# Kernel tuning notes

Hardware: AMD Instinct MI355X
Metric: run time of the kernel (lower is better)

The kernel has to match this reference:

```python
import jax, jax.numpy as jnp
import numpy as np

N_NODES = 50000
N_EDGES = 800000
D = 128


def gcn_conv(x, W, b, src, dst, num_nodes):
    """PyG GCNConv: x @ W, add self-loops, symmetric normalization, scatter-add, + bias."""
    x = x @ W  # [N, out]
    loop = jnp.arange(num_nodes, dtype=src.dtype)
    s = jnp.concatenate([src, loop])  # [E+N]
    d = jnp.concatenate([dst, loop])
    w = jnp.ones(s.shape[0], x.dtype)  # edge_weight=None -> ones (self-loop fill=1)
    deg = jax.ops.segment_sum(w, d, num_segments=num_nodes)  # [N]
    dinv = jnp.where(deg > 0, jax.lax.rsqrt(deg), 0.0)
    norm = dinv[s] * dinv[d]  # [E+N]
    out = jax.ops.segment_sum(x[s] * norm[:, None], d, num_segments=num_nodes)
    return out + b


def setup_inputs() -> dict:
    key = jax.random.key(0)
    ks = jax.random.split(key, 8)
    sc = 1.0 / np.sqrt(D)
    x = jax.random.normal(ks[0], (N_NODES, D), dtype=jnp.float32)
    edge_index = jax.random.randint(ks[1], (2, N_EDGES), 0, N_NODES)
    W1 = jax.random.normal(ks[2], (D, D), dtype=jnp.float32) * sc
    W2 = jax.random.normal(ks[3], (D, D), dtype=jnp.float32) * sc
    W3 = jax.random.normal(ks[4], (D, D), dtype=jnp.float32) * sc
    b1 = jnp.zeros((D,), jnp.float32)
    b2 = jnp.zeros((D,), jnp.float32)
    b3 = jnp.zeros((D,), jnp.float32)
    return {"x": x, "edge_index": edge_index, "W1": W1, "b1": b1,
            "W2": W2, "b2": b2, "W3": W3, "b3": b3}


def reference(x, edge_index, W1, b1, W2, b2, W3, b3):
    src, dst = edge_index[0], edge_index[1]
    n = x.shape[0]
    x = jax.nn.relu(gcn_conv(x, W1, b1, src, dst, n))
    x = jax.nn.relu(gcn_conv(x, W2, b2, src, dst, n))
    return gcn_conv(x, W3, b3, src, dst, n)
```

## Files before the change

kernel.cpp:

```cpp
#include <hip/hip_runtime.h>
#include <hip/hip_fp16.h>
#include <math.h>

#define D 128

typedef __attribute__((ext_vector_type(8))) _Float16 half8;
typedef __attribute__((ext_vector_type(4))) float f32x4;


__global__ void count_rank_kernel(const int* __restrict__ dst, int* __restrict__ cnt,
                                  int* __restrict__ rank, int E) {
    int e0 = (blockIdx.x * blockDim.x + threadIdx.x) * 8;
    if (e0 + 7 < E) {
        int4 da = *(const int4*)(dst + e0);
        int4 db = *(const int4*)(dst + e0 + 4);
        int4 ra, rb;
        ra.x = atomicAdd(&cnt[da.x], 1);
        ra.y = atomicAdd(&cnt[da.y], 1);
        ra.z = atomicAdd(&cnt[da.z], 1);
        ra.w = atomicAdd(&cnt[da.w], 1);
        rb.x = atomicAdd(&cnt[db.x], 1);
        rb.y = atomicAdd(&cnt[db.y], 1);
        rb.z = atomicAdd(&cnt[db.z], 1);
        rb.w = atomicAdd(&cnt[db.w], 1);
        *(int4*)(rank + e0)     = ra;
        *(int4*)(rank + e0 + 4) = rb;
    } else {
        for (int e = e0; e < E; ++e) rank[e] = atomicAdd(&cnt[dst[e]], 1);
    }
}

__global__ __launch_bounds__(1024) void scan_kernel(const int* __restrict__ cnt,
                                                    int* __restrict__ rowptr,
                                                    float* __restrict__ dinv,
                                                    int N) {
    __shared__ int wsum[16];
    __shared__ int carry_s;
    int tid  = threadIdx.x;
    int lane = tid & 63;
    int wid  = tid >> 6;
    if (tid == 0) carry_s = 0;
    __syncthreads();
    for (int base = 0; base < N; base += 4096) {
        int i = base + tid * 4;
        int4 v = make_int4(0, 0, 0, 0);
        if (i + 3 < N) v = *(const int4*)(cnt + i);
        else {
            if (i + 0 < N) v.x = cnt[i + 0];
            if (i + 1 < N) v.y = cnt[i + 1];
            if (i + 2 < N) v.z = cnt[i + 2];
            if (i + 3 < N) v.w = cnt[i + 3];
        }
        int s0 = v.x, s1 = s0 + v.y, s2 = s1 + v.z, s3 = s2 + v.w;
        int sc = s3;
        #pragma unroll
        for (int off = 1; off < 64; off <<= 1) {
            int t = __shfl_up(sc, off, 64);
            if (lane >= off) sc += t;
        }
        if (lane == 63) wsum[wid] = sc;
        __syncthreads();
        if (tid < 16) {
            int w = wsum[tid];
            #pragma unroll
            for (int off = 1; off < 16; off <<= 1) {
                int t = __shfl_up(w, off, 64);
                if (tid >= off) w += t;
            }
            wsum[tid] = w;
        }
        __syncthreads();
        int waveoff = (wid > 0) ? wsum[wid - 1] : 0;
        int excl = carry_s + waveoff + (sc - s3);
        if (i + 0 < N) { rowptr[i + 0] = excl;      dinv[i + 0] = rsqrtf((float)v.x + 1.0f); }
        if (i + 1 < N) { rowptr[i + 1] = excl + s0; dinv[i + 1] = rsqrtf((float)v.y + 1.0f); }
        if (i + 2 < N) { rowptr[i + 2] = excl + s1; dinv[i + 2] = rsqrtf((float)v.z + 1.0f); }
        if (i + 3 < N) { rowptr[i + 3] = excl + s2; dinv[i + 3] = rsqrtf((float)v.w + 1.0f); }
        __syncthreads();
        if (tid == 0) carry_s += wsum[15];
        __syncthreads();
    }
    if (tid == 0) rowptr[N] = carry_s;
}

__global__ void fill_kernel(const int* __restrict__ src, const int* __restrict__ dst,
                            const int* __restrict__ rank, const int* __restrict__ rowptr,
                            int* __restrict__ col, int E) {
    int e0 = (blockIdx.x * blockDim.x + threadIdx.x) * 8;
    if (e0 + 7 < E) {
        int4 da = *(const int4*)(dst + e0);
        int4 db = *(const int4*)(dst + e0 + 4);
        int4 ra = *(const int4*)(rank + e0);
        int4 rb = *(const int4*)(rank + e0 + 4);
        int4 sa = *(const int4*)(src + e0);
        int4 sb = *(const int4*)(src + e0 + 4);
        int p0 = rowptr[da.x] + ra.x;
        int p1 = rowptr[da.y] + ra.y;
        int p2 = rowptr[da.z] + ra.z;
        int p3 = rowptr[da.w] + ra.w;
        int p4 = rowptr[db.x] + rb.x;
        int p5 = rowptr[db.y] + rb.y;
        int p6 = rowptr[db.z] + rb.z;
        int p7 = rowptr[db.w] + rb.w;
        col[p0] = sa.x; col[p1] = sa.y; col[p2] = sa.z; col[p3] = sa.w;
        col[p4] = sb.x; col[p5] = sb.y; col[p6] = sb.z; col[p7] = sb.w;
    } else {
        for (int e = e0; e < E; ++e) col[rowptr[dst[e]] + rank[e]] = src[e];
    }
}


__global__ void convw_kernel(const float* __restrict__ W1, const float* __restrict__ W2,
                             const float* __restrict__ W3, __half* __restrict__ WhT) {
    int i = blockIdx.x * blockDim.x + threadIdx.x;
    int l = i >> 14;
    int j = i & 16383;
    int n = j >> 7, k = j & 127;
    const float* W = (l == 0) ? W1 : (l == 1) ? W2 : W3;
    WhT[(size_t)i] = __float2half(W[(size_t)k * D + n]);
}


__global__ __launch_bounds__(256) void gemm_mfma_f32(const float* __restrict__ X,
                                                     const __half* __restrict__ WhT,
                                                     const float* __restrict__ dinv,
                                                     __half* __restrict__ Y, int M) {
    int tid  = threadIdx.x;
    int wave = tid >> 6;
    int lane = tid & 63;
    int quad = lane >> 4;
    int l16  = lane & 15;
    int m0   = blockIdx.x * 64 + wave * 16;
    if (m0 >= M) return;

    f32x4 acc[8];
    #pragma unroll
    for (int t = 0; t < 8; ++t) acc[t] = (f32x4)0.0f;

    const float* xrow = X + (size_t)(m0 + l16) * D;

    #pragma unroll
    for (int ks = 0; ks < 4; ++ks) {
        int k0 = ks * 32 + quad * 8;
        float4 x0 = *(const float4*)(xrow + k0);
        float4 x1 = *(const float4*)(xrow + k0 + 4);
        half8 a;
        a[0] = (_Float16)x0.x; a[1] = (_Float16)x0.y;
        a[2] = (_Float16)x0.z; a[3] = (_Float16)x0.w;
        a[4] = (_Float16)x1.x; a[5] = (_Float16)x1.y;
        a[6] = (_Float16)x1.z; a[7] = (_Float16)x1.w;
        #pragma unroll
        for (int t = 0; t < 8; ++t) {
            half8 b = *(const half8*)(WhT + (size_t)(t * 16 + l16) * D + k0);
            acc[t] = __builtin_amdgcn_mfma_f32_16x16x32_f16(a, b, acc[t], 0, 0, 0);
        }
    }

    float4 dv = *(const float4*)(dinv + m0 + quad * 4);
    float dvs[4] = {dv.x, dv.y, dv.z, dv.w};
    #pragma unroll
    for (int t = 0; t < 8; ++t) {
        #pragma unroll
        for (int r = 0; r < 4; ++r) {
            int grow = m0 + quad * 4 + r;
            Y[(size_t)grow * D + t * 16 + l16] = __float2half(acc[t][r] * dvs[r]);
        }
    }
}

__global__ __launch_bounds__(256) void gemm_mfma_f16(const __half* __restrict__ Xh,
                                                     const __half* __restrict__ WhT,
                                                     const float* __restrict__ dinv,
                                                     __half* __restrict__ Y, int M) {
    int tid  = threadIdx.x;
    int wave = tid >> 6;
    int lane = tid & 63;
    int quad = lane >> 4;
    int l16  = lane & 15;
    int m0   = blockIdx.x * 64 + wave * 16;
    if (m0 >= M) return;

    f32x4 acc[8];
    #pragma unroll
    for (int t = 0; t < 8; ++t) acc[t] = (f32x4)0.0f;

    const __half* xrow = Xh + (size_t)(m0 + l16) * D;

    #pragma unroll
    for (int ks = 0; ks < 4; ++ks) {
        int k0 = ks * 32 + quad * 8;
        half8 a = *(const half8*)(xrow + k0);
        #pragma unroll
        for (int t = 0; t < 8; ++t) {
            half8 b = *(const half8*)(WhT + (size_t)(t * 16 + l16) * D + k0);
            acc[t] = __builtin_amdgcn_mfma_f32_16x16x32_f16(a, b, acc[t], 0, 0, 0);
        }
    }

    float4 dv = *(const float4*)(dinv + m0 + quad * 4);
    float dvs[4] = {dv.x, dv.y, dv.z, dv.w};
    #pragma unroll
    for (int t = 0; t < 8; ++t) {
        #pragma unroll
        for (int r = 0; r < 4; ++r) {
            int grow = m0 + quad * 4 + r;
            Y[(size_t)grow * D + t * 16 + l16] = __float2half(acc[t][r] * dvs[r]);
        }
    }
}


#define GATHER(vv, cc) __half2 vv = ((const __half2*)(ys + (size_t)(cc) * D))[lane]

template <bool FINAL>
__global__ __launch_bounds__(256) void aggregate_kernel(const __half* __restrict__ ys,
                                                        const int* __restrict__ rowptr,
                                                        const int* __restrict__ col,
                                                        const float* __restrict__ dinv,
                                                        const float* __restrict__ b,
                                                        __half* __restrict__ outh,
                                                        float* __restrict__ outf,
                                                        int N) {
    int gwave = (blockIdx.x * blockDim.x + threadIdx.x) >> 6;
    int lane  = threadIdx.x & 63;
    if (gwave >= N) return;
    int row = gwave;
    int s = rowptr[row], e = rowptr[row + 1];

    __half2 hself = ((const __half2*)(ys + (size_t)row * D))[lane];
    float2 a0 = __half22float2(hself);
    float2 a1 = make_float2(0.f, 0.f), a2 = make_float2(0.f, 0.f),
           a3 = make_float2(0.f, 0.f), a4 = make_float2(0.f, 0.f),
           a5 = make_float2(0.f, 0.f), a6 = make_float2(0.f, 0.f),
           a7 = make_float2(0.f, 0.f);

    for (int base = s; base < e; base += 64) {
        int idx = base + lane;
        int myc = (idx < e) ? col[idx] : 0;
        int nb  = min(64, e - base);
        int j = 0;
        for (; j + 16 <= nb; j += 16) {
            int c0 = __shfl(myc, j + 0),  c1 = __shfl(myc, j + 1);
            int c2 = __shfl(myc, j + 2),  c3 = __shfl(myc, j + 3);
            int c4 = __shfl(myc, j + 4),  c5 = __shfl(myc, j + 5);
            int c6 = __shfl(myc, j + 6),  c7 = __shfl(myc, j + 7);
            int c8 = __shfl(myc, j + 8),  c9 = __shfl(myc, j + 9);
            int cA = __shfl(myc, j + 10), cB = __shfl(myc, j + 11);
            int cC = __shfl(myc, j + 12), cD = __shfl(myc, j + 13);
            int cE = __shfl(myc, j + 14), cF = __shfl(myc, j + 15);
            GATHER(v0, c0); GATHER(v1, c1); GATHER(v2, c2); GATHER(v3, c3);
            GATHER(v4, c4); GATHER(v5, c5); GATHER(v6, c6); GATHER(v7, c7);
            GATHER(v8, c8); GATHER(v9, c9); GATHER(vA, cA); GATHER(vB, cB);
            GATHER(vC, cC); GATHER(vD, cD); GATHER(vE, cE); GATHER(vF, cF);
            a0.x += __low2float(v0); a0.y += __high2float(v0);
            a1.x += __low2float(v1); a1.y += __high2float(v1);
            a2.x += __low2float(v2); a2.y += __high2float(v2);
            a3.x += __low2float(v3); a3.y += __high2float(v3);
            a4.x += __low2float(v4); a4.y += __high2float(v4);
            a5.x += __low2float(v5); a5.y += __high2float(v5);
            a6.x += __low2float(v6); a6.y += __high2float(v6);
            a7.x += __low2float(v7); a7.y += __high2float(v7);
            a0.x += __low2float(v8); a0.y += __high2float(v8);
            a1.x += __low2float(v9); a1.y += __high2float(v9);
            a2.x += __low2float(vA); a2.y += __high2float(vA);
            a3.x += __low2float(vB); a3.y += __high2float(vB);
            a4.x += __low2float(vC); a4.y += __high2float(vC);
            a5.x += __low2float(vD); a5.y += __high2float(vD);
            a6.x += __low2float(vE); a6.y += __high2float(vE);
            a7.x += __low2float(vF); a7.y += __high2float(vF);
        }
        for (; j + 8 <= nb; j += 8) {
            int c0 = __shfl(myc, j + 0), c1 = __shfl(myc, j + 1);
            int c2 = __shfl(myc, j + 2), c3 = __shfl(myc, j + 3);
            int c4 = __shfl(myc, j + 4), c5 = __shfl(myc, j + 5);
            int c6 = __shfl(myc, j + 6), c7 = __shfl(myc, j + 7);
            GATHER(v0, c0); GATHER(v1, c1); GATHER(v2, c2); GATHER(v3, c3);
            GATHER(v4, c4); GATHER(v5, c5); GATHER(v6, c6); GATHER(v7, c7);
            a0.x += __low2float(v0); a0.y += __high2float(v0);
            a1.x += __low2float(v1); a1.y += __high2float(v1);
            a2.x += __low2float(v2); a2.y += __high2float(v2);
            a3.x += __low2float(v3); a3.y += __high2float(v3);
            a4.x += __low2float(v4); a4.y += __high2float(v4);
            a5.x += __low2float(v5); a5.y += __high2float(v5);
            a6.x += __low2float(v6); a6.y += __high2float(v6);
            a7.x += __low2float(v7); a7.y += __high2float(v7);
        }
        for (; j + 4 <= nb; j += 4) {
            int c0 = __shfl(myc, j + 0), c1 = __shfl(myc, j + 1);
            int c2 = __shfl(myc, j + 2), c3 = __shfl(myc, j + 3);
            GATHER(v0, c0); GATHER(v1, c1); GATHER(v2, c2); GATHER(v3, c3);
            a0.x += __low2float(v0); a0.y += __high2float(v0);
            a1.x += __low2float(v1); a1.y += __high2float(v1);
            a2.x += __low2float(v2); a2.y += __high2float(v2);
            a3.x += __low2float(v3); a3.y += __high2float(v3);
        }
        for (; j < nb; ++j) {
            int c = __shfl(myc, j);
            GATHER(v, c);
            a0.x += __low2float(v); a0.y += __high2float(v);
        }
    }
    a0.x += a1.x + a2.x + a3.x + a4.x + a5.x + a6.x + a7.x;
    a0.y += a1.y + a2.y + a3.y + a4.y + a5.y + a6.y + a7.y;

    float dv  = dinv[row];
    float2 bb = ((const float2*)b)[lane];
    float rx = bb.x + dv * a0.x;
    float ry = bb.y + dv * a0.y;
    if (FINAL) {
        ((float2*)(outf + (size_t)row * D))[lane] = make_float2(rx, ry);
    } else {
        __half2 hv = __floats2half2_rn(fmaxf(rx, 0.f), fmaxf(ry, 0.f));
        ((__half2*)(outh + (size_t)row * D))[lane] = hv;
    }
}


extern "C" void kernel_launch(void* const* d_in, const int* in_sizes, int n_in,
                              void* d_out, int out_size, void* d_ws, size_t ws_size,
                              hipStream_t stream) {
    const float* x   = (const float*)d_in[0];
    const int*   ei  = (const int*)d_in[1];
    const float* W1  = (const float*)d_in[2];
    const float* b1  = (const float*)d_in[3];
    const float* W2  = (const float*)d_in[4];
    const float* b2  = (const float*)d_in[5];
    const float* W3  = (const float*)d_in[6];
    const float* b3  = (const float*)d_in[7];
    float* out = (float*)d_out;

    const int N = in_sizes[0] / D;
    const int E = in_sizes[1] / 2;
    const int* src = ei;
    const int* dst = ei + E;

    char* ws = (char*)d_ws;
    size_t off = 0;
    auto alloc = [&](size_t bytes) {
        void* p = ws + off;
        off = (off + bytes + 255) & ~(size_t)255;
        return p;
    };
    __half* ys    = (__half*)alloc((size_t)N * D * sizeof(__half));
    __half* hs    = (__half*)alloc((size_t)N * D * sizeof(__half));
    int*   cnt    = (int*)alloc((size_t)N * sizeof(int));
    int*   rowptr = (int*)alloc((size_t)(N + 1) * sizeof(int));
    float* dinv   = (float*)alloc((size_t)N * sizeof(float));
    int*   rank   = (int*)alloc((size_t)E * sizeof(int));
    int*   col    = (int*)alloc((size_t)E * sizeof(int));
    __half* WhT   = (__half*)alloc((size_t)3 * D * D * sizeof(__half));
    (void)ws_size; (void)n_in; (void)out_size;

    convw_kernel<<<(3 * D * D + 255) / 256, 256, 0, stream>>>(W1, W2, W3, WhT);

    hipMemsetAsync(cnt, 0, (size_t)N * sizeof(int), stream);
    const int egrid = ((E + 7) / 8 + 255) / 256;
    count_rank_kernel<<<egrid, 256, 0, stream>>>(dst, cnt, rank, E);
    scan_kernel<<<1, 1024, 0, stream>>>(cnt, rowptr, dinv, N);
    fill_kernel<<<egrid, 256, 0, stream>>>(src, dst, rank, rowptr, col, E);

    const int gemm_grid = (N + 63) / 64;
    const int agg_grid  = (N * 64 + 255) / 256;

    gemm_mfma_f32<<<gemm_grid, 256, 0, stream>>>(x, WhT, dinv, ys, N);
    aggregate_kernel<false><<<agg_grid, 256, 0, stream>>>(ys, rowptr, col, dinv, b1, hs, nullptr, N);
    gemm_mfma_f16<<<gemm_grid, 256, 0, stream>>>(hs, WhT + 16384, dinv, ys, N);
    aggregate_kernel<false><<<agg_grid, 256, 0, stream>>>(ys, rowptr, col, dinv, b2, hs, nullptr, N);
    gemm_mfma_f16<<<gemm_grid, 256, 0, stream>>>(hs, WhT + 32768, dinv, ys, N);
    aggregate_kernel<true><<<agg_grid, 256, 0, stream>>>(ys, rowptr, col, dinv, b3, nullptr, out, N);
}
```

Measured before the change: 332.6 us.

## Fuse aggregation with next-layer GEMM via LDS and merge setup kernels

Each layer's neighbor aggregation is fused with the following layer's MFMA GEMM: every wave gathers 16 rows, applies bias, ReLU and fp16 conversion into padded LDS, then multiplies them by the next weight matrix. This removes the fp16 intermediate round-trip through global memory and two kernel launches. The CSR fill is merged with the first GEMM into one heterogeneous grid, and the weight conversion is merged with zeroing the counter array. The cost is lower parallelism in aggregation: each wave now walks 16 rows in sequence where before there was one wave per row, so gather latency hiding may suffer.

```diff
diff --git a/kernel.cpp b/kernel.cpp
--- a/kernel.cpp
+++ b/kernel.cpp
@@ -3,9 +3,25 @@
 #include <math.h>
 
 #define D 128
+#define PADH 136
 
 typedef __attribute__((ext_vector_type(8))) _Float16 half8;
 typedef __attribute__((ext_vector_type(4))) float f32x4;
+
+
+__global__ void prep_kernel(const float* __restrict__ W1, const float* __restrict__ W2,
+                            const float* __restrict__ W3, __half* __restrict__ WhT,
+                            int* __restrict__ cnt, int N) {
+    int i = blockIdx.x * blockDim.x + threadIdx.x;
+    if (i < 3 * D * D) {
+        int l = i >> 14;
+        int j = i & 16383;
+        int n = j >> 7, k = j & 127;
+        const float* W = (l == 0) ? W1 : (l == 1) ? W2 : W3;
+        WhT[(size_t)i] = __float2half(W[(size_t)k * D + n]);
+    }
+    if (i < N) cnt[i] = 0;
+}
 
 
 __global__ void count_rank_kernel(const int* __restrict__ dst, int* __restrict__ cnt,
@@ -83,151 +99,15 @@
     if (tid == 0) rowptr[N] = carry_s;
 }
 
-__global__ void fill_kernel(const int* __restrict__ src, const int* __restrict__ dst,
-                            const int* __restrict__ rank, const int* __restrict__ rowptr,
-                            int* __restrict__ col, int E) {
-    int e0 = (blockIdx.x * blockDim.x + threadIdx.x) * 8;
-    if (e0 + 7 < E) {
-        int4 da = *(const int4*)(dst + e0);
-        int4 db = *(const int4*)(dst + e0 + 4);
-        int4 ra = *(const int4*)(rank + e0);
-        int4 rb = *(const int4*)(rank + e0 + 4);
-        int4 sa = *(const int4*)(src + e0);
-        int4 sb = *(const int4*)(src + e0 + 4);
-        int p0 = rowptr[da.x] + ra.x;
-        int p1 = rowptr[da.y] + ra.y;
-        int p2 = rowptr[da.z] + ra.z;
-        int p3 = rowptr[da.w] + ra.w;
-        int p4 = rowptr[db.x] + rb.x;
-        int p5 = rowptr[db.y] + rb.y;
-        int p6 = rowptr[db.z] + rb.z;
-        int p7 = rowptr[db.w] + rb.w;
-        col[p0] = sa.x; col[p1] = sa.y; col[p2] = sa.z; col[p3] = sa.w;
-        col[p4] = sb.x; col[p5] = sb.y; col[p6] = sb.z; col[p7] = sb.w;
-    } else {
-        for (int e = e0; e < E; ++e) col[rowptr[dst[e]] + rank[e]] = src[e];
-    }
-}
-
-
-__global__ void convw_kernel(const float* __restrict__ W1, const float* __restrict__ W2,
-                             const float* __restrict__ W3, __half* __restrict__ WhT) {
-    int i = blockIdx.x * blockDim.x + threadIdx.x;
-    int l = i >> 14;
-    int j = i & 16383;
-    int n = j >> 7, k = j & 127;
-    const float* W = (l == 0) ? W1 : (l == 1) ? W2 : W3;
-    WhT[(size_t)i] = __float2half(W[(size_t)k * D + n]);
-}
-
-
-__global__ __launch_bounds__(256) void gemm_mfma_f32(const float* __restrict__ X,
-                                                     const __half* __restrict__ WhT,
-                                                     const float* __restrict__ dinv,
-                                                     __half* __restrict__ Y, int M) {
-    int tid  = threadIdx.x;
-    int wave = tid >> 6;
-    int lane = tid & 63;
-    int quad = lane >> 4;
-    int l16  = lane & 15;
-    int m0   = blockIdx.x * 64 + wave * 16;
-    if (m0 >= M) return;
-
-    f32x4 acc[8];
-    #pragma unroll
-    for (int t = 0; t < 8; ++t) acc[t] = (f32x4)0.0f;
-
-    const float* xrow = X + (size_t)(m0 + l16) * D;
-
-    #pragma unroll
-    for (int ks = 0; ks < 4; ++ks) {
-        int k0 = ks * 32 + quad * 8;
-        float4 x0 = *(const float4*)(xrow + k0);
-        float4 x1 = *(const float4*)(xrow + k0 + 4);
-        half8 a;
-        a[0] = (_Float16)x0.x; a[1] = (_Float16)x0.y;
-        a[2] = (_Float16)x0.z; a[3] = (_Float16)x0.w;
-        a[4] = (_Float16)x1.x; a[5] = (_Float16)x1.y;
-        a[6] = (_Float16)x1.z; a[7] = (_Float16)x1.w;
-        #pragma unroll
-        for (int t = 0; t < 8; ++t) {
-            half8 b = *(const half8*)(WhT + (size_t)(t * 16 + l16) * D + k0);
-            acc[t] = __builtin_amdgcn_mfma_f32_16x16x32_f16(a, b, acc[t], 0, 0, 0);
-        }
-    }
-
-    float4 dv = *(const float4*)(dinv + m0 + quad * 4);
-    float dvs[4] = {dv.x, dv.y, dv.z, dv.w};
-    #pragma unroll
-    for (int t = 0; t < 8; ++t) {
-        #pragma unroll
-        for (int r = 0; r < 4; ++r) {
-            int grow = m0 + quad * 4 + r;
-            Y[(size_t)grow * D + t * 16 + l16] = __float2half(acc[t][r] * dvs[r]);
-        }
-    }
-}
-
-__global__ __launch_bounds__(256) void gemm_mfma_f16(const __half* __restrict__ Xh,
-                                                     const __half* __restrict__ WhT,
-                                                     const float* __restrict__ dinv,
-                                                     __half* __restrict__ Y, int M) {
-    int tid  = threadIdx.x;
-    int wave = tid >> 6;
-    int lane = tid & 63;
-    int quad = lane >> 4;
-    int l16  = lane & 15;
-    int m0   = blockIdx.x * 64 + wave * 16;
-    if (m0 >= M) return;
-
-    f32x4 acc[8];
-    #pragma unroll
-    for (int t = 0; t < 8; ++t) acc[t] = (f32x4)0.0f;
-
-    const __half* xrow = Xh + (size_t)(m0 + l16) * D;
-
-    #pragma unroll
-    for (int ks = 0; ks < 4; ++ks) {
-        int k0 = ks * 32 + quad * 8;
-        half8 a = *(const half8*)(xrow + k0);
-        #pragma unroll
-        for (int t = 0; t < 8; ++t) {
-            half8 b = *(const half8*)(WhT + (size_t)(t * 16 + l16) * D + k0);
-            acc[t] = __builtin_amdgcn_mfma_f32_16x16x32_f16(a, b, acc[t], 0, 0, 0);
-        }
-    }
-
-    float4 dv = *(const float4*)(dinv + m0 + quad * 4);
-    float dvs[4] = {dv.x, dv.y, dv.z, dv.w};
-    #pragma unroll
-    for (int t = 0; t < 8; ++t) {
-        #pragma unroll
-        for (int r = 0; r < 4; ++r) {
-            int grow = m0 + quad * 4 + r;
-            Y[(size_t)grow * D + t * 16 + l16] = __float2half(acc[t][r] * dvs[r]);
-        }
-    }
-}
-
-
-#define GATHER(vv, cc) __half2 vv = ((const __half2*)(ys + (size_t)(cc) * D))[lane]
-
-template <bool FINAL>
-__global__ __launch_bounds__(256) void aggregate_kernel(const __half* __restrict__ ys,
-                                                        const int* __restrict__ rowptr,
-                                                        const int* __restrict__ col,
-                                                        const float* __restrict__ dinv,
-                                                        const float* __restrict__ b,
-                                                        __half* __restrict__ outh,
-                                                        float* __restrict__ outf,
-                                                        int N) {
-    int gwave = (blockIdx.x * blockDim.x + threadIdx.x) >> 6;
-    int lane  = threadIdx.x & 63;
-    if (gwave >= N) return;
-    int row = gwave;
+
+#define GATHER(vv, cc) __half2 vv = ((const __half2*)(g + (size_t)(cc) * D))[lane]
+
+__device__ __forceinline__ float2 gather_row(const __half* __restrict__ g,
+                                             const int* __restrict__ rowptr,
+                                             const int* __restrict__ col,
+                                             int row, int lane) {
     int s = rowptr[row], e = rowptr[row + 1];
-
-    __half2 hself = ((const __half2*)(ys + (size_t)row * D))[lane];
+    __half2 hself = ((const __half2*)(g + (size_t)row * D))[lane];
     float2 a0 = __half22float2(hself);
     float2 a1 = make_float2(0.f, 0.f), a2 = make_float2(0.f, 0.f),
            a3 = make_float2(0.f, 0.f), a4 = make_float2(0.f, 0.f),
@@ -302,17 +182,156 @@
     }
     a0.x += a1.x + a2.x + a3.x + a4.x + a5.x + a6.x + a7.x;
     a0.y += a1.y + a2.y + a3.y + a4.y + a5.y + a6.y + a7.y;
-
-    float dv  = dinv[row];
+    return a0;
+}
+
+
+__global__ __launch_bounds__(256) void fill_gemm1_kernel(
+    const int* __restrict__ src, const int* __restrict__ dst,
+    const int* __restrict__ rank, const int* __restrict__ rowptr,
+    int* __restrict__ col, int E, int fill_blocks,
+    const float* __restrict__ X, const __half* __restrict__ WhT,
+    const float* __restrict__ dinv, __half* __restrict__ Y, int M) {
+    int tid = threadIdx.x;
+    if ((int)blockIdx.x < fill_blocks) {
+        int e0 = (blockIdx.x * 256 + tid) * 8;
+        if (e0 + 7 < E) {
+            int4 da = *(const int4*)(dst + e0);
+            int4 db = *(const int4*)(dst + e0 + 4);
+            int4 ra = *(const int4*)(rank + e0);
+            int4 rb = *(const int4*)(rank + e0 + 4);
+            int4 sa = *(const int4*)(src + e0);
+            int4 sb = *(const int4*)(src + e0 + 4);
+            int p0 = rowptr[da.x] + ra.x;
+            int p1 = rowptr[da.y] + ra.y;
+            int p2 = rowptr[da.z] + ra.z;
+            int p3 = rowptr[da.w] + ra.w;
+            int p4 = rowptr[db.x] + rb.x;
+            int p5 = rowptr[db.y] + rb.y;
+            int p6 = rowptr[db.z] + rb.z;
+            int p7 = rowptr[db.w] + rb.w;
+            col[p0] = sa.x; col[p1] = sa.y; col[p2] = sa.z; col[p3] = sa.w;
+            col[p4] = sb.x; col[p5] = sb.y; col[p6] = sb.z; col[p7] = sb.w;
+        } else {
+            for (int e = e0; e < E; ++e) col[rowptr[dst[e]] + rank[e]] = src[e];
+        }
+        return;
+    }
+    int bid  = blockIdx.x - fill_blocks;
+    int wave = tid >> 6;
+    int lane = tid & 63;
+    int quad = lane >> 4;
+    int l16  = lane & 15;
+    int m0   = bid * 64 + wave * 16;
+    if (m0 >= M) return;
+
+    f32x4 acc[8];
+    #pragma unroll
+    for (int t = 0; t < 8; ++t) acc[t] = (f32x4)0.0f;
+
+    const float* xrow = X + (size_t)(m0 + l16) * D;
+
+    #pragma unroll
+    for (int ks = 0; ks < 4; ++ks) {
+        int k0 = ks * 32 + quad * 8;
+        float4 x0 = *(const float4*)(xrow + k0);
+        float4 x1 = *(const float4*)(xrow + k0 + 4);
+        half8 a;
+        a[0] = (_Float16)x0.x; a[1] = (_Float16)x0.y;
+        a[2] = (_Float16)x0.z; a[3] = (_Float16)x0.w;
+        a[4] = (_Float16)x1.x; a[5] = (_Float16)x1.y;
+        a[6] = (_Float16)x1.z; a[7] = (_Float16)x1.w;
+        #pragma unroll
+        for (int t = 0; t < 8; ++t) {
+            half8 b = *(const half8*)(WhT + (size_t)(t * 16 + l16) * D + k0);
+            acc[t] = __builtin_amdgcn_mfma_f32_16x16x32_f16(a, b, acc[t], 0, 0, 0);
+        }
+    }
+
+    float4 dv = *(const float4*)(dinv + m0 + quad * 4);
+    float dvs[4] = {dv.x, dv.y, dv.z, dv.w};
+    #pragma unroll
+    for (int t = 0; t < 8; ++t) {
+        #pragma unroll
+        for (int r = 0; r < 4; ++r) {
+            int grow = m0 + quad * 4 + r;
+            Y[(size_t)grow * D + t * 16 + l16] = __float2half(acc[t][r] * dvs[r]);
+        }
+    }
+}
+
+
+__global__ __launch_bounds__(256) void agg_gemm_kernel(
+    const __half* __restrict__ ysIn, const int* __restrict__ rowptr,
+    const int* __restrict__ col, const float* __restrict__ dinv,
+    const float* __restrict__ bias, const __half* __restrict__ WhT,
+    __half* __restrict__ ysOut, int M) {
+    __shared__ __half lds_h[64 * PADH];
+    int tid  = threadIdx.x;
+    int wave = tid >> 6;
+    int lane = tid & 63;
+    int rbase = blockIdx.x * 64 + wave * 16;
+
+    float2 bb = ((const float2*)bias)[lane];
+    for (int t = 0; t < 16; ++t) {
+        int row = rbase + t;
+        if (row < M) {
+            float2 a = gather_row(ysIn, rowptr, col, row, lane);
+            float dv = dinv[row];
+            float rx = bb.x + dv * a.x;
+            float ry = bb.y + dv * a.y;
+            __half2 hv = __floats2half2_rn(fmaxf(rx, 0.f), fmaxf(ry, 0.f));
+            ((__half2*)(lds_h + (size_t)(wave * 16 + t) * PADH))[lane] = hv;
+        }
+    }
+    __syncthreads();
+
+    int quad = lane >> 4;
+    int l16  = lane & 15;
+    int m0   = rbase;
+    if (m0 >= M) return;
+
+    f32x4 acc[8];
+    #pragma unroll
+    for (int t = 0; t < 8; ++t) acc[t] = (f32x4)0.0f;
+
+    const __half* arow = lds_h + (size_t)(wave * 16 + l16) * PADH;
+
+    #pragma unroll
+    for (int ks = 0; ks < 4; ++ks) {
+        int k0 = ks * 32 + quad * 8;
+        half8 a = *(const half8*)(arow + k0);
+        #pragma unroll
+        for (int t = 0; t < 8; ++t) {
+            half8 b = *(const half8*)(WhT + (size_t)(t * 16 + l16) * D + k0);
+            acc[t] = __builtin_amdgcn_mfma_f32_16x16x32_f16(a, b, acc[t], 0, 0, 0);
+        }
+    }
+
+    float4 dv = *(const float4*)(dinv + m0 + quad * 4);
+    float dvs[4] = {dv.x, dv.y, dv.z, dv.w};
+    #pragma unroll
+    for (int t = 0; t < 8; ++t) {
+        #pragma unroll
+        for (int r = 0; r < 4; ++r) {
+            int grow = m0 + quad * 4 + r;
+            ysOut[(size_t)grow * D + t * 16 + l16] = __float2half(acc[t][r] * dvs[r]);
+        }
+    }
+}
+
+
+__global__ __launch_bounds__(256) void agg_final_kernel(
+    const __half* __restrict__ ys, const int* __restrict__ rowptr,
+    const int* __restrict__ col, const float* __restrict__ dinv,
+    const float* __restrict__ b, float* __restrict__ out, int N) {
+    int gwave = (blockIdx.x * blockDim.x + threadIdx.x) >> 6;
+    int lane  = threadIdx.x & 63;
+    if (gwave >= N) return;
+    float2 a  = gather_row(ys, rowptr, col, gwave, lane);
+    float dv  = dinv[gwave];
     float2 bb = ((const float2*)b)[lane];
-    float rx = bb.x + dv * a0.x;
-    float ry = bb.y + dv * a0.y;
-    if (FINAL) {
-        ((float2*)(outf + (size_t)row * D))[lane] = make_float2(rx, ry);
-    } else {
-        __half2 hv = __floats2half2_rn(fmaxf(rx, 0.f), fmaxf(ry, 0.f));
-        ((__half2*)(outh + (size_t)row * D))[lane] = hv;
-    }
+    ((float2*)(out + (size_t)gwave * D))[lane] = make_float2(bb.x + dv * a.x, bb.y + dv * a.y);
 }
 
 
@@ -351,21 +370,20 @@
     __half* WhT   = (__half*)alloc((size_t)3 * D * D * sizeof(__half));
     (void)ws_size; (void)n_in; (void)out_size;
 
-    convw_kernel<<<(3 * D * D + 255) / 256, 256, 0, stream>>>(W1, W2, W3, WhT);
-
-    hipMemsetAsync(cnt, 0, (size_t)N * sizeof(int), stream);
+    int prep_threads = (3 * D * D > N) ? 3 * D * D : N;
+    prep_kernel<<<(prep_threads + 255) / 256, 256, 0, stream>>>(W1, W2, W3, WhT, cnt, N);
+
     const int egrid = ((E + 7) / 8 + 255) / 256;
     count_rank_kernel<<<egrid, 256, 0, stream>>>(dst, cnt, rank, E);
     scan_kernel<<<1, 1024, 0, stream>>>(cnt, rowptr, dinv, N);
-    fill_kernel<<<egrid, 256, 0, stream>>>(src, dst, rank, rowptr, col, E);
 
     const int gemm_grid = (N + 63) / 64;
-    const int agg_grid  = (N * 64 + 255) / 256;
-
-    gemm_mfma_f32<<<gemm_grid, 256, 0, stream>>>(x, WhT, dinv, ys, N);
-    aggregate_kernel<false><<<agg_grid, 256, 0, stream>>>(ys, rowptr, col, dinv, b1, hs, nullptr, N);
-    gemm_mfma_f16<<<gemm_grid, 256, 0, stream>>>(hs, WhT + 16384, dinv, ys, N);
-    aggregate_kernel<false><<<agg_grid, 256, 0, stream>>>(ys, rowptr, col, dinv, b2, hs, nullptr, N);
-    gemm_mfma_f16<<<gemm_grid, 256, 0, stream>>>(hs, WhT + 32768, dinv, ys, N);
-    aggregate_kernel<true><<<agg_grid, 256, 0, stream>>>(ys, rowptr, col, dinv, b3, nullptr, out, N);
-}
+    fill_gemm1_kernel<<<egrid + gemm_grid, 256, 0, stream>>>(
+        src, dst, rank, rowptr, col, E, egrid, x, WhT, dinv, ys, N);
+
+    agg_gemm_kernel<<<gemm_grid, 256, 0, stream>>>(ys, rowptr, col, dinv, b1, WhT + 16384, hs, N);
+    agg_gemm_kernel<<<gemm_grid, 256, 0, stream>>>(hs, rowptr, col, dinv, b2, WhT + 32768, ys, N);
+
+    const int agg_grid = (N * 64 + 255) / 256;
+    agg_final_kernel<<<agg_grid, 256, 0, stream>>>(ys, rowptr, col, dinv, b3, out, N);
+}
```

After: 332.5 us. No clear change (-0.0%).
